# Kernel optimization log

Hardware: AMD Instinct MI355X
Metric: run time of the kernel (lower is better)

## Reference

```python
import jax, jax.numpy as jnp
import numpy as np

# dims (see shape_source)
B, N, P, H, M, E, HOPS = 512, 102, 12, 256, 4, 3, 2
C_CLIP = 10.0   # logit clipping constant params['C']
T = 1.0         # temperature params['T']
NEG = -1e9


def setup_inputs() -> dict:
    key = jax.random.key(0)
    ks = jax.random.split(key, 18)
    s = 0.08  # uniform init range as in _initialize_weights, use scaled normals
    inp = {
        "node_features": jax.random.normal(ks[0], (B, N, P), jnp.float32),
        "adjacency": jax.random.uniform(ks[1], (B, E, N, N), jnp.float32),  # per-edge-cat weighted adjacency
        "mask": jax.random.randint(ks[2], (B, N), 0, 2).astype(jnp.int32),  # 1 = already scheduled / forbidden
        # encoder params
        "W_emb": jax.random.normal(ks[3], (P, H), jnp.float32) * s,
        "W_rel": jax.random.normal(ks[4], (HOPS, E, H, H), jnp.float32) * s / np.sqrt(H),
        "W_self": jax.random.normal(ks[5], (HOPS, H, H), jnp.float32) * s / np.sqrt(H),
        # multi-head glimpse params (Vec / W_q / W_ref per head)
        "Vec": jax.random.normal(ks[6], (M, H, H), jnp.float32) * s,
        "W_q": jax.random.normal(ks[7], (M, 3 * H, H), jnp.float32) * s,
        "W_ref": jax.random.normal(ks[8], (M, H, H), jnp.float32) * s,
        "W_mh": jax.random.normal(ks[9], (M * H, H), jnp.float32) * s,  # multi_head_embedding
        # final pointer params
        "Vec2": jax.random.normal(ks[10], (H,), jnp.float32) * s,
        "W_q2": jax.random.normal(ks[11], (H, H), jnp.float32) * s,
        "W_ref2": jax.random.normal(ks[12], (H, H), jnp.float32) * s,
        # learned decoder seed vectors
        "dec_input": jax.random.normal(ks[13], (H,), jnp.float32) * s,
        "v_1": jax.random.normal(ks[14], (H,), jnp.float32) * s,
    }
    return inp


def reference(node_features, adjacency, mask, W_emb, W_rel, W_self, Vec, W_q,
              W_ref, W_mh, Vec2, W_q2, W_ref2, dec_input, v_1):
    # ---- encoder: linear embedding + HOPS of relational (per-edge-category) message passing ----
    h = jnp.einsum('bnp,ph->bnh', node_features, W_emb)            # [B,N,H]
    for hop in range(HOPS):
        msg = jnp.einsum('benm,bmh->benh', adjacency, h)           # gather neighbors per edge cat
        h = jax.nn.relu(jnp.einsum('benh,ehk->bnk', msg, W_rel[hop])
                        + jnp.einsum('bnh,hk->bnk', h, W_self[hop]))
    enc = h                                                         # [B,N,H]

    # ---- decoder query: cat(graph readout, learned dec_input, learned v_1) -> 3H ----
    enc_mean = enc.mean(axis=1)                                     # [B,H]
    q_cat = jnp.concatenate([enc_mean,
                             jnp.broadcast_to(dec_input, (B, H)),
                             jnp.broadcast_to(v_1, (B, H))], axis=-1)  # [B,3H]

    # ---- multi-head additive (Bahdanau) glimpse: per-head Vec/W_q/W_ref tanh scoring ----
    q = jnp.einsum('bf,mfh->bmh', q_cat, W_q)                       # [B,M,H]
    r = jnp.einsum('bnh,mhk->bmnk', enc, W_ref)                     # [B,M,N,H]
    u = jnp.einsum('bmnh,mhk->bmnk', jnp.tanh(q[:, :, None, :] + r), Vec)
    scores = u.sum(axis=-1)                                         # [B,M,N]
    scores = jnp.where(mask[:, None, :] > 0, NEG, scores)
    a = jax.nn.softmax(scores, axis=-1)
    ctx = jnp.einsum('bmn,bnh->bmh', a, enc).reshape(B, M * H)
    query2 = ctx @ W_mh                                             # [B,H]

    # ---- final pointer head (Vec2 / W_q2 / W_ref2) ----
    u2 = jnp.einsum('h,bnh->bn', Vec2,
                    jnp.tanh((query2 @ W_q2)[:, None, :] + jnp.einsum('bnh,hk->bnk', enc, W_ref2)))
    u2 = C_CLIP * jnp.tanh(u2)                                      # logit clipping
    u2 = jnp.where(mask > 0, NEG, u2)
    log_p = jax.nn.log_softmax(u2 / T, axis=-1)                     # [B,N]
    return log_p
```

## Files before the change

kernel.cpp:

```cpp
#include <hip/hip_runtime.h>
#include <hip/hip_bf16.h>

#define B 512
#define N 102
#define Pdim 12
#define H 256
#define M 4
#define E 3
#define NEG (-1e9f)
#define RT 52224
#define NN 10404

typedef __hip_bfloat16 bf16;
typedef __attribute__((ext_vector_type(8))) short short8;
typedef __attribute__((ext_vector_type(4))) float f32x4;
typedef __attribute__((ext_vector_type(16))) float f32x16;

__device__ __forceinline__ float b2f(bf16 v) { return __bfloat162float(v); }
__device__ __forceinline__ bf16 f2b(float v) { return __float2bfloat16(v); }
__device__ __forceinline__ short f2bs(float v) {
    bf16 t = __float2bfloat16(v);
    return *reinterpret_cast<short*>(&t);
}
__device__ __forceinline__ float fast_tanh(float x) {
    float e = __expf(2.f * x);
    return 1.f - 2.f * __builtin_amdgcn_rcpf(e + 1.f);
}
__device__ __forceinline__ void gload_lds4(const unsigned int* g, unsigned int* l) {
    __builtin_amdgcn_global_load_lds(
        (const __attribute__((address_space(1))) unsigned int*)g,
        (__attribute__((address_space(3))) unsigned int*)l, 4, 0, 0);
}

__global__ __launch_bounds__(256) void wt_prep(const float* __restrict__ Wrel,
                                               const float* __restrict__ Wself,
                                               const float* __restrict__ Wref,
                                               const float* __restrict__ Wref2,
                                               const float* __restrict__ Wmh,
                                               const float* __restrict__ Wq2,
                                               const float* __restrict__ W_q,
                                               const float* __restrict__ Vec,
                                               const float* __restrict__ W_emb,
                                               const float* __restrict__ dec,
                                               const float* __restrict__ v1,
                                               const float* __restrict__ adj,
                                               short* __restrict__ wfrag,
                                               short* __restrict__ wrefT,
                                               short* __restrict__ wref2T,
                                               short* __restrict__ wmh_bf,
                                               short* __restrict__ wq2_bf,
                                               short* __restrict__ wq_bf,
                                               short* __restrict__ wembf,
                                               short* __restrict__ adjp,
                                               float* __restrict__ qconst,
                                               float* __restrict__ vsum) {
    int bid = blockIdx.x;
    int tid = threadIdx.x;
    __shared__ short tl[1024 * 17];
    if (bid >= 3652) {
        int be = bid - 3652;
        const float* src = adj + (size_t)be * NN;
        short* dst = adjp + (size_t)be * (112 * 128);
        for (int i = tid; i < 112 * 128; i += 256) {
            int n = i >> 7, m = i & 127;
            short v = 0;
            if (n < N && m < N) v = f2bs(src[n * N + m]);
            dst[i] = v;
        }
        return;
    }
    if (bid < 32) {
        int hop = bid >> 4, ct = bid & 15;
        for (int i = tid; i < 16384; i += 256) {
            int k = i >> 4, c0 = i & 15;
            int c = ct * 16 + c0;
            float v;
            if (k < 768) v = Wrel[(((size_t)hop * E + (k >> 8)) * H + (k & 255)) * H + c];
            else         v = Wself[((size_t)hop * H + (k - 768)) * H + c];
            tl[k * 17 + c0] = f2bs(v);
        }
        __syncthreads();
        short8* outp = (short8*)wfrag + (size_t)(hop * 16 + ct) * 2048;
        for (int i = tid; i < 2048; i += 256) {
            int ks = i >> 6, lq = i & 63;
            int c0 = lq & 15, kb = (lq >> 4) * 8;
            short8 v;
#pragma unroll
            for (int j = 0; j < 8; ++j) v[j] = tl[(ks * 32 + kb + j) * 17 + c0];
            outp[i] = v;
        }
        return;
    }
    if (bid >= 3648) {
        int m = bid - 3648, hh = tid;
        __shared__ float dls[H], vls[H];
        dls[hh] = dec[hh];
        vls[hh] = v1[hh];
        __syncthreads();
        const float* Wm = W_q + (size_t)m * (3 * H) * H;
        float s = 0.f;
        for (int f = 0; f < H; ++f)
            s += dls[f] * Wm[(H + f) * H + hh] + vls[f] * Wm[(2 * H + f) * H + hh];
        qconst[m * H + hh] = s;
        float vs = 0.f;
        const float* Vr = Vec + ((size_t)m * H + hh) * H;
        for (int k = 0; k < H; ++k) vs += Vr[k];
        vsum[m * H + hh] = vs;
        return;
    }
    int idx = 524288 + (bid - 32) * 256 + tid;
    if (idx < 786432) {
        int r = idx - 524288;
        int row = r >> 8, k = r & 255;
        int m = row >> 8, c = row & 255;
        wrefT[r] = f2bs(Wref[((size_t)m * H + k) * H + c]);
    } else if (idx < 851968) {
        int r = idx - 786432;
        int c = r >> 8, k = r & 255;
        wref2T[r] = f2bs(Wref2[k * H + c]);
    } else if (idx < 1114112) {
        int r = idx - 851968;
        wmh_bf[r] = f2bs(Wmh[r]);
    } else if (idx < 1179648) {
        int r = idx - 1114112;
        wq2_bf[r] = f2bs(Wq2[r]);
    } else if (idx < 1441792) {
        int r = idx - 1179648;
        int m = r >> 16, fh = r & 65535;
        wq_bf[r] = f2bs(W_q[(size_t)m * 768 * 256 + fh]);
    } else if (idx < 1449984) {
        int r = idx - 1441792;
        int ct = r >> 9, lq = (r >> 3) & 63, j = r & 7;
        int c = ct * 16 + (lq & 15), k = (lq >> 4) * 8 + j;
        wembf[r] = (k < Pdim) ? f2bs(W_emb[k * H + c]) : (short)0;
    }
}

#define HP 264
#define YP2 136
#define ASP 136
__global__ __launch_bounds__(512, 2) void enc_fused(const float* __restrict__ nf,
                                                    const short* __restrict__ wembf,
                                                    const short* __restrict__ adjp,
                                                    const short* __restrict__ wfragp,
                                                    bf16* __restrict__ enc_out,
                                                    float* __restrict__ mean_out) {
    int b = blockIdx.x;
    int tid = threadIdx.x;
    int w = tid >> 6;
    int l = tid & 63;
    int cg = l & 15;
    int rg = l >> 4;
    int ct0 = 2 * w, ct1 = ct0 + 1;

    __shared__ short hS[112 * HP];
    __shared__ short YtS[256 * YP2];
    __shared__ short AsS[112 * ASP];

    const short8 z8 = {0, 0, 0, 0, 0, 0, 0, 0};
    for (int i = tid; i < 10 * 32; i += 512) {
        int n = 102 + (i >> 5), g = i & 31;
        *(short8*)(&hS[n * HP + g * 8]) = z8;
    }
    {
        int c = tid >> 1, g = 14 + (tid & 1);
        *(short8*)(&YtS[c * YP2 + g * 8]) = z8;
    }

    {
        const short8* we8 = (const short8*)wembf;
        short8 bfe0 = we8[ct0 * 64 + l];
        short8 bfe1 = we8[ct1 * 64 + l];
#pragma unroll
        for (int nt = 0; nt < 7; ++nt) {
            int row = nt * 16 + cg;
            short8 afr = z8;
            if (row < 102 && rg < 2) {
                const float* src = nf + ((size_t)b * N + row) * Pdim + rg * 8;
                f32x4 v0 = *(const f32x4*)src;
                afr[0] = f2bs(v0[0]); afr[1] = f2bs(v0[1]);
                afr[2] = f2bs(v0[2]); afr[3] = f2bs(v0[3]);
                if (rg == 0) {
                    f32x4 v1 = *(const f32x4*)(src + 4);
                    afr[4] = f2bs(v1[0]); afr[5] = f2bs(v1[1]);
                    afr[6] = f2bs(v1[2]); afr[7] = f2bs(v1[3]);
                }
            }
            f32x4 d0 = (f32x4){0.f, 0.f, 0.f, 0.f}, d1 = d0;
            d0 = __builtin_amdgcn_mfma_f32_16x16x32_bf16(afr, bfe0, d0, 0, 0, 0);
            d1 = __builtin_amdgcn_mfma_f32_16x16x32_bf16(afr, bfe1, d1, 0, 0, 0);
#pragma unroll
            for (int r = 0; r < 4; ++r) {
                int n = nt * 16 + rg * 4 + r;
                hS[n * HP + ct0 * 16 + cg] = f2bs(d0[r]);
                hS[n * HP + ct1 * 16 + cg] = f2bs(d1[r]);
            }
        }
    }
    __syncthreads();

    for (int hop = 0; hop < 2; ++hop) {
        const short8* wf8 = ((const short8*)wfragp) + (size_t)hop * 32768;
        f32x4 hacc0[7], hacc1[7];
#pragma unroll
        for (int j = 0; j < 7; ++j) {
            hacc0[j] = (f32x4){0.f, 0.f, 0.f, 0.f};
            hacc1[j] = hacc0[j];
        }

        for (int estep = 0; estep < E; ++estep) {
            int e = hop ? (2 - estep) : estep;
            if (!(hop == 1 && estep == 0)) {
                const short* Abase = adjp + (size_t)(b * E + e) * 14336;
#pragma unroll
                for (int j = 0; j < 14; ++j) {
                    int n = w * 14 + j;
                    const unsigned int* gsrc = (const unsigned int*)(Abase + n * 128) + l;
                    gload_lds4(gsrc, (unsigned int*)&AsS[n * ASP]);
                }
            }
            if (estep == 0) {
#pragma unroll
                for (int ks = 0; ks < 8; ++ks) {
                    short8 wfs0 = wf8[(ct0 * 32 + 24 + ks) * 64 + l];
                    short8 wfs1 = wf8[(ct1 * 32 + 24 + ks) * 64 + l];
#pragma unroll
                    for (int nt = 0; nt < 7; ++nt) {
                        short8 hf = *(const short8*)(&hS[(nt * 16 + cg) * HP + ks * 32 + rg * 8]);
                        hacc0[nt] = __builtin_amdgcn_mfma_f32_16x16x32_bf16(hf, wfs0, hacc0[nt], 0, 0, 0);
                        hacc1[nt] = __builtin_amdgcn_mfma_f32_16x16x32_bf16(hf, wfs1, hacc1[nt], 0, 0, 0);
                    }
                }
            }
            f32x4 g0[7], g1[7];
#pragma unroll
            for (int j = 0; j < 7; ++j) {
                g0[j] = (f32x4){0.f, 0.f, 0.f, 0.f};
                g1[j] = g0[j];
            }
#pragma unroll
            for (int ks = 0; ks < 8; ++ks) {
                short8 wfa0 = wf8[(ct0 * 32 + e * 8 + ks) * 64 + l];
                short8 wfa1 = wf8[(ct1 * 32 + e * 8 + ks) * 64 + l];
#pragma unroll
                for (int mt = 0; mt < 7; ++mt) {
                    short8 hf = *(const short8*)(&hS[(mt * 16 + cg) * HP + ks * 32 + rg * 8]);
                    g0[mt] = __builtin_amdgcn_mfma_f32_16x16x32_bf16(wfa0, hf, g0[mt], 0, 0, 0);
                    g1[mt] = __builtin_amdgcn_mfma_f32_16x16x32_bf16(wfa1, hf, g1[mt], 0, 0, 0);
                }
            }
#pragma unroll
            for (int mt = 0; mt < 7; ++mt)
#pragma unroll
                for (int r = 0; r < 4; ++r) {
                    int c0 = ct0 * 16 + rg * 4 + r;
                    int c1 = ct1 * 16 + rg * 4 + r;
                    YtS[c0 * YP2 + mt * 16 + cg] = f2bs(g0[mt][r]);
                    YtS[c1 * YP2 + mt * 16 + cg] = f2bs(g1[mt][r]);
                }
            __syncthreads();
#pragma unroll
            for (int ks = 0; ks < 4; ++ks) {
                short8 yf0 = *(const short8*)(&YtS[(ct0 * 16 + cg) * YP2 + (ks * 4 + rg) * 8]);
                short8 yf1 = *(const short8*)(&YtS[(ct1 * 16 + cg) * YP2 + (ks * 4 + rg) * 8]);
#pragma unroll
                for (int nt = 0; nt < 7; ++nt) {
                    short8 af = *(const short8*)(&AsS[(nt * 16 + cg) * ASP + ks * 32 + rg * 8]);
                    hacc0[nt] = __builtin_amdgcn_mfma_f32_16x16x32_bf16(af, yf0, hacc0[nt], 0, 0, 0);
                    hacc1[nt] = __builtin_amdgcn_mfma_f32_16x16x32_bf16(af, yf1, hacc1[nt], 0, 0, 0);
                }
            }
            __syncthreads();
        }
#pragma unroll
        for (int nt = 0; nt < 7; ++nt)
#pragma unroll
            for (int r = 0; r < 4; ++r) {
                int n = nt * 16 + rg * 4 + r;
                float v0 = hacc0[nt][r], v1 = hacc1[nt][r];
                hS[n * HP + ct0 * 16 + cg] = f2bs(v0 > 0.f ? v0 : 0.f);
                hS[n * HP + ct1 * 16 + cg] = f2bs(v1 > 0.f ? v1 : 0.f);
            }
        __syncthreads();
    }

    short* ho = (short*)enc_out;
    for (int i = tid; i < 102 * 32; i += 512) {
        int n = i >> 5, g = i & 31;
        *(short8*)(ho + ((size_t)b * N + n) * H + g * 8) = *(const short8*)(&hS[n * HP + g * 8]);
    }
    {
        float* partf = (float*)AsS;
        int c = tid & 255, qq = tid >> 8;
        float s = 0.f;
        for (int n = qq; n < N; n += 2) s += b2f(*(const bf16*)&hS[n * HP + c]);
        partf[qq * 256 + c] = s;
        __syncthreads();
        if (tid < 256)
            mean_out[(size_t)b * H + tid] = (partf[tid] + partf[256 + tid]) * (1.f / (float)N);
    }
}

__global__ __launch_bounds__(256, 2) void head2_mfma(const bf16* __restrict__ X,
                                                     const short* __restrict__ WT,
                                                     const float* __restrict__ qb, int qbs,
                                                     const float* __restrict__ vsb,
                                                     float* __restrict__ outp, int obs,
                                                     int mcnt) {
    int rt = blockIdx.x;
    int r0 = rt * 128;
    int tid = threadIdx.x;
    int w = tid >> 6, l = tid & 63;
    int lr = l & 31;
    int lh = l >> 5;
    __shared__ short Xs[128 * 256];
    __shared__ float qls[12 * 256];
    __shared__ float part[4][128];

    const short* Xp = (const short*)X;
#pragma unroll
    for (int i = 0; i < 16; ++i) {
        int id = tid + i * 256;
        int r = id >> 5, g = id & 31;
        short8 v = *(const short8*)(Xp + (size_t)(r0 + r) * H + g * 8);
        *(short8*)((char*)Xs + r * 512 + ((g ^ (r & 7)) * 16)) = v;
    }
    int b_base = r0 / N;
    for (int i = tid; i < 3 * mcnt * 256; i += 256) {
        int boff = i / (mcnt * 256);
        int rem = i - boff * (mcnt * 256);
        int m = rem >> 8, c = rem & 255;
        int bb = b_base + boff;
        if (bb > B - 1) bb = B - 1;
        qls[(boff * mcnt + m) * 256 + c] = qb[(size_t)bb * qbs + m * H + c];
    }
    __syncthreads();

    int swz = lr & 7;
    for (int m = 0; m < mcnt; ++m) {
        const short8* w8 = (const short8*)(WT + (size_t)m * H * H);
        int cbase = w * 64;
        short8 afr0[16], afr1[16];
#pragma unroll
        for (int ks = 0; ks < 16; ++ks) {
            afr0[ks] = w8[(size_t)(cbase + lr) * 32 + ks * 2 + lh];
            afr1[ks] = w8[(size_t)(cbase + 32 + lr) * 32 + ks * 2 + lh];
        }
        float vsl[32];
#pragma unroll
        for (int j = 0; j < 16; ++j) {
            int cl = (j & 3) + 8 * (j >> 2) + 4 * lh;
            vsl[j]      = vsb[m * H + w * 64 + cl];
            vsl[16 + j] = vsb[m * H + w * 64 + 32 + cl];
        }
        for (int t = 0; t < 4; ++t) {
            f32x16 acc0, acc1;
#pragma unroll
            for (int j = 0; j < 16; ++j) { acc0[j] = 0.f; acc1[j] = 0.f; }
            const char* xbase = (const char*)Xs + (t * 32 + lr) * 512;
#pragma unroll
            for (int ks = 0; ks < 16; ++ks) {
                short8 bx = *(const short8*)(xbase + (((2 * ks + lh) ^ swz) * 16));
                acc0 = __builtin_amdgcn_mfma_f32_32x32x16_bf16(afr0[ks], bx, acc0, 0, 0, 0);
                acc1 = __builtin_amdgcn_mfma_f32_32x32x16_bf16(afr1[ks], bx, acc1, 0, 0, 0);
            }
            int r = r0 + t * 32 + lr;
            int b = r / N;
            int boff = b - b_base;
            const float* qrow = &qls[(boff * mcnt + m) * 256];
            float s = 0.f;
#pragma unroll
            for (int j = 0; j < 16; ++j) {
                int cl = (j & 3) + 8 * (j >> 2) + 4 * lh;
                float x0 = qrow[w * 64 + cl] + acc0[j];
                s += fast_tanh(x0) * vsl[j];
                float x1 = qrow[w * 64 + 32 + cl] + acc1[j];
                s += fast_tanh(x1) * vsl[16 + j];
            }
            s += __shfl_xor(s, 32, 64);
            if (l < 32) part[w][t * 32 + lr] = s;
        }
        __syncthreads();
        if (tid < 128) {
            int r = r0 + tid;
            int b = r / N, n = r - b * N;
            outp[(size_t)b * obs + m * N + n] = part[0][tid] + part[1][tid] + part[2][tid] + part[3][tid];
        }
        __syncthreads();
    }
}

__global__ __launch_bounds__(256) void q_k(const float* __restrict__ enc_mean,
                                           const short* __restrict__ wq_bf,
                                           const float* __restrict__ qconst,
                                           float* __restrict__ qbuf) {
    int bid = blockIdx.x;
    int b = bid >> 2, m = bid & 3;
    int hh = threadIdx.x;
    __shared__ float em[H];
    em[hh] = enc_mean[(size_t)b * H + hh];
    __syncthreads();
    const bf16* Wm = (const bf16*)(wq_bf + (size_t)m * 65536);
    float s = qconst[m * H + hh];
    for (int f = 0; f < H; ++f) s += em[f] * b2f(Wm[f * H + hh]);
    qbuf[((size_t)b * M + m) * H + hh] = s;
}

__global__ __launch_bounds__(256) void dec_mid_k(const float* __restrict__ scores,
                                                 const int* __restrict__ mask,
                                                 const bf16* __restrict__ enc,
                                                 const short* __restrict__ wmh,
                                                 const short* __restrict__ wq2,
                                                 float* __restrict__ q2) {
    int b = blockIdx.x;
    int tid = threadIdx.x;
    int w = tid >> 6;
    int l = tid & 63;
    __shared__ short hEnc[102 * 264];
    __shared__ float a[M][112];
    __shared__ float red[M];
    __shared__ float cx[M * H];
    __shared__ float qy[H];

    const short* ep = (const short*)enc;
    for (int i = tid; i < 102 * 32; i += 256) {
        int n = i >> 5, g = i & 31;
        *(short8*)(&hEnc[n * 264 + g * 8]) = *(const short8*)(ep + ((size_t)b * N + n) * H + g * 8);
    }
    for (int i = tid; i < M * 112; i += 256) {
        int m = i / 112, n = i % 112;
        float s = NEG;
        if (n < N) s = (mask[(size_t)b * N + n] > 0) ? NEG : scores[((size_t)b * M + m) * N + n];
        a[m][n] = s;
    }
    __syncthreads();
    {
        float v = a[w][l];
        float v2 = (l + 64 < 112) ? a[w][l + 64] : NEG;
        v = fmaxf(v, v2);
        v = fmaxf(v, __shfl_xor(v, 32, 64));
        v = fmaxf(v, __shfl_xor(v, 16, 64));
        v = fmaxf(v, __shfl_xor(v, 8, 64));
        v = fmaxf(v, __shfl_xor(v, 4, 64));
        v = fmaxf(v, __shfl_xor(v, 2, 64));
        v = fmaxf(v, __shfl_xor(v, 1, 64));
        float mx = __shfl(v, 0, 64);
        float e0 = __expf(a[w][l] - mx);
        float e1 = (l + 64 < 112) ? __expf(a[w][l + 64] - mx) : 0.f;
        a[w][l] = e0;
        if (l + 64 < 112) a[w][l + 64] = e1;
        float sv = e0 + e1;
        sv += __shfl_xor(sv, 32, 64);
        sv += __shfl_xor(sv, 16, 64);
        sv += __shfl_xor(sv, 8, 64);
        sv += __shfl_xor(sv, 4, 64);
        sv += __shfl_xor(sv, 2, 64);
        sv += __shfl_xor(sv, 1, 64);
        if (l == 0) red[w] = __builtin_amdgcn_rcpf(sv);
    }
    __syncthreads();
    float c0 = 0.f, c1 = 0.f, c2 = 0.f, c3 = 0.f;
    for (int n = 0; n < N; ++n) {
        float e = b2f(*(const bf16*)&hEnc[n * 264 + tid]);
        c0 += a[0][n] * e;
        c1 += a[1][n] * e;
        c2 += a[2][n] * e;
        c3 += a[3][n] * e;
    }
    cx[0 * H + tid] = c0 * red[0];
    cx[1 * H + tid] = c1 * red[1];
    cx[2 * H + tid] = c2 * red[2];
    cx[3 * H + tid] = c3 * red[3];
    __syncthreads();
    const bf16* wm = (const bf16*)wmh;
    float acc = 0.f;
    for (int j = 0; j < M * H; ++j) acc += cx[j] * b2f(wm[(size_t)j * H + tid]);
    qy[tid] = acc;
    __syncthreads();
    const bf16* w2 = (const bf16*)wq2;
    float acc2 = 0.f;
    for (int k = 0; k < H; ++k) acc2 += qy[k] * b2f(w2[(size_t)k * H + tid]);
    q2[(size_t)b * H + tid] = acc2;
}

__global__ __launch_bounds__(128) void final_out_k(const float* __restrict__ u2,
                                                   const int* __restrict__ mask,
                                                   float* __restrict__ out) {
    int b = blockIdx.x;
    int tid = threadIdx.x;
    __shared__ float a[128];
    __shared__ float red[2];
    float u = NEG;
    if (tid < N) {
        u = 10.f * fast_tanh(u2[(size_t)b * N + tid]);
        if (mask[(size_t)b * N + tid] > 0) u = NEG;
    }
    a[tid] = u;
    __syncthreads();
    if (tid < 64) {
        float v = fmaxf(a[tid], a[tid + 64]);
        v = fmaxf(v, __shfl_xor(v, 32, 64));
        v = fmaxf(v, __shfl_xor(v, 16, 64));
        v = fmaxf(v, __shfl_xor(v, 8, 64));
        v = fmaxf(v, __shfl_xor(v, 4, 64));
        v = fmaxf(v, __shfl_xor(v, 2, 64));
        v = fmaxf(v, __shfl_xor(v, 1, 64));
        if (tid == 0) red[0] = v;
    }
    __syncthreads();
    float mx = red[0];
    float ev = (tid < N) ? __expf(u - mx) : 0.f;
    a[tid] = ev;
    __syncthreads();
    if (tid < 64) {
        float v = a[tid] + a[tid + 64];
        v += __shfl_xor(v, 32, 64);
        v += __shfl_xor(v, 16, 64);
        v += __shfl_xor(v, 8, 64);
        v += __shfl_xor(v, 4, 64);
        v += __shfl_xor(v, 2, 64);
        v += __shfl_xor(v, 1, 64);
        if (tid == 0) red[1] = logf(v);
    }
    __syncthreads();
    if (tid < N) out[(size_t)b * N + tid] = (u - mx) - red[1];
}

extern "C" void kernel_launch(void* const* d_in, const int* in_sizes, int n_in,
                              void* d_out, int out_size, void* d_ws, size_t ws_size,
                              hipStream_t stream) {
    const float* nf     = (const float*)d_in[0];
    const float* adj    = (const float*)d_in[1];
    const int*   mask   = (const int*)d_in[2];
    const float* W_emb  = (const float*)d_in[3];
    const float* W_rel  = (const float*)d_in[4];
    const float* W_self = (const float*)d_in[5];
    const float* Vec    = (const float*)d_in[6];
    const float* W_q    = (const float*)d_in[7];
    const float* W_ref  = (const float*)d_in[8];
    const float* W_mh   = (const float*)d_in[9];
    const float* Vec2   = (const float*)d_in[10];
    const float* W_q2   = (const float*)d_in[11];
    const float* W_ref2 = (const float*)d_in[12];
    const float* dec    = (const float*)d_in[13];
    const float* v_1    = (const float*)d_in[14];
    float* out = (float*)d_out;

    char* p = (char*)d_ws;
    size_t off = 0;
    auto alloc = [&](size_t bytes) -> char* {
        char* q = p + off;
        off += (bytes + 255) & ~(size_t)255;
        return q;
    };
    bf16* hA      = (bf16*)alloc((size_t)RT * H * sizeof(bf16));
    short* adjp   = (short*)alloc((size_t)B * E * 112 * 128 * sizeof(short));
    short* wfrag  = (short*)alloc(524288 * sizeof(short));
    short* wrefT  = (short*)alloc(262144 * sizeof(short));
    short* wref2T = (short*)alloc(65536 * sizeof(short));
    short* wmh_bf = (short*)alloc(262144 * sizeof(short));
    short* wq2_bf = (short*)alloc(65536 * sizeof(short));
    short* wq_bf  = (short*)alloc(262144 * sizeof(short));
    short* wembf  = (short*)alloc(8192 * sizeof(short));
    float* enc_mean = (float*)alloc((size_t)B * H * sizeof(float));
    float* qconst   = (float*)alloc((size_t)M * H * sizeof(float));
    float* vsumb    = (float*)alloc((size_t)M * H * sizeof(float));
    float* qbuf     = (float*)alloc((size_t)B * M * H * sizeof(float));
    float* scoresb  = (float*)alloc((size_t)B * M * N * sizeof(float));
    float* q2b      = (float*)alloc((size_t)B * H * sizeof(float));
    float* u2b      = (float*)alloc((size_t)B * N * sizeof(float));

    wt_prep<<<5188, 256, 0, stream>>>(W_rel, W_self, W_ref, W_ref2, W_mh, W_q2,
                                      W_q, Vec, W_emb, dec, v_1, adj,
                                      wfrag, wrefT, wref2T, wmh_bf, wq2_bf, wq_bf, wembf,
                                      adjp, qconst, vsumb);

    enc_fused<<<B, 512, 0, stream>>>(nf, wembf, adjp, wfrag, hA, enc_mean);

    const bf16* enc = hA;

    q_k<<<B * M, 256, 0, stream>>>(enc_mean, wq_bf, qconst, qbuf);
    head2_mfma<<<RT / 128, 256, 0, stream>>>(enc, wrefT, qbuf, M * H, vsumb, scoresb, M * N, M);
    dec_mid_k<<<B, 256, 0, stream>>>(scoresb, mask, enc, wmh_bf, wq2_bf, q2b);
    head2_mfma<<<RT / 128, 256, 0, stream>>>(enc, wref2T, q2b, H, Vec2, u2b, N, 1);
    final_out_k<<<B, 128, 0, stream>>>(u2b, mask, out);
}
```

Before: 266.2 us.

## Fuse decoder glimpse, context, pointer head and log-softmax into one per-batch kernel

Replaces four decoder kernels (two head2_mfma launches, dec_mid_k, final_out_k) with one dec_fused kernel, one block per batch element. The encoder tile is loaded into LDS once and reused for the multi-head scoring MFMAs, the context reduction and the final pointer MFMAs, which removes the intermediate scores, q2 and u2 round-trips through global memory and three launches. In exchange, each block pads 102 rows to 128, so a quarter of the MFMA work is wasted. The grid is also 512 blocks instead of 408, and the serial per-thread W_mh/W_q2 matvecs now sit inside the same kernel as the MFMA work.

Measured after the change: 282.2 us. 6.0% more time.

```diff
diff --git a/kernel.cpp b/kernel.cpp
--- a/kernel.cpp
+++ b/kernel.cpp
@@ -301,95 +301,6 @@
     }
 }
 
-__global__ __launch_bounds__(256, 2) void head2_mfma(const bf16* __restrict__ X,
-                                                     const short* __restrict__ WT,
-                                                     const float* __restrict__ qb, int qbs,
-                                                     const float* __restrict__ vsb,
-                                                     float* __restrict__ outp, int obs,
-                                                     int mcnt) {
-    int rt = blockIdx.x;
-    int r0 = rt * 128;
-    int tid = threadIdx.x;
-    int w = tid >> 6, l = tid & 63;
-    int lr = l & 31;
-    int lh = l >> 5;
-    __shared__ short Xs[128 * 256];
-    __shared__ float qls[12 * 256];
-    __shared__ float part[4][128];
-
-    const short* Xp = (const short*)X;
-#pragma unroll
-    for (int i = 0; i < 16; ++i) {
-        int id = tid + i * 256;
-        int r = id >> 5, g = id & 31;
-        short8 v = *(const short8*)(Xp + (size_t)(r0 + r) * H + g * 8);
-        *(short8*)((char*)Xs + r * 512 + ((g ^ (r & 7)) * 16)) = v;
-    }
-    int b_base = r0 / N;
-    for (int i = tid; i < 3 * mcnt * 256; i += 256) {
-        int boff = i / (mcnt * 256);
-        int rem = i - boff * (mcnt * 256);
-        int m = rem >> 8, c = rem & 255;
-        int bb = b_base + boff;
-        if (bb > B - 1) bb = B - 1;
-        qls[(boff * mcnt + m) * 256 + c] = qb[(size_t)bb * qbs + m * H + c];
-    }
-    __syncthreads();
-
-    int swz = lr & 7;
-    for (int m = 0; m < mcnt; ++m) {
-        const short8* w8 = (const short8*)(WT + (size_t)m * H * H);
-        int cbase = w * 64;
-        short8 afr0[16], afr1[16];
-#pragma unroll
-        for (int ks = 0; ks < 16; ++ks) {
-            afr0[ks] = w8[(size_t)(cbase + lr) * 32 + ks * 2 + lh];
-            afr1[ks] = w8[(size_t)(cbase + 32 + lr) * 32 + ks * 2 + lh];
-        }
-        float vsl[32];
-#pragma unroll
-        for (int j = 0; j < 16; ++j) {
-            int cl = (j & 3) + 8 * (j >> 2) + 4 * lh;
-            vsl[j]      = vsb[m * H + w * 64 + cl];
-            vsl[16 + j] = vsb[m * H + w * 64 + 32 + cl];
-        }
-        for (int t = 0; t < 4; ++t) {
-            f32x16 acc0, acc1;
-#pragma unroll
-            for (int j = 0; j < 16; ++j) { acc0[j] = 0.f; acc1[j] = 0.f; }
-            const char* xbase = (const char*)Xs + (t * 32 + lr) * 512;
-#pragma unroll
-            for (int ks = 0; ks < 16; ++ks) {
-                short8 bx = *(const short8*)(xbase + (((2 * ks + lh) ^ swz) * 16));
-                acc0 = __builtin_amdgcn_mfma_f32_32x32x16_bf16(afr0[ks], bx, acc0, 0, 0, 0);
-                acc1 = __builtin_amdgcn_mfma_f32_32x32x16_bf16(afr1[ks], bx, acc1, 0, 0, 0);
-            }
-            int r = r0 + t * 32 + lr;
-            int b = r / N;
-            int boff = b - b_base;
-            const float* qrow = &qls[(boff * mcnt + m) * 256];
-            float s = 0.f;
-#pragma unroll
-            for (int j = 0; j < 16; ++j) {
-                int cl = (j & 3) + 8 * (j >> 2) + 4 * lh;
-                float x0 = qrow[w * 64 + cl] + acc0[j];
-                s += fast_tanh(x0) * vsl[j];
-                float x1 = qrow[w * 64 + 32 + cl] + acc1[j];
-                s += fast_tanh(x1) * vsl[16 + j];
-            }
-            s += __shfl_xor(s, 32, 64);
-            if (l < 32) part[w][t * 32 + lr] = s;
-        }
-        __syncthreads();
-        if (tid < 128) {
-            int r = r0 + tid;
-            int b = r / N, n = r - b * N;
-            outp[(size_t)b * obs + m * N + n] = part[0][tid] + part[1][tid] + part[2][tid] + part[3][tid];
-        }
-        __syncthreads();
-    }
-}
-
 __global__ __launch_bounds__(256) void q_k(const float* __restrict__ enc_mean,
                                            const short* __restrict__ wq_bf,
                                            const float* __restrict__ qconst,
@@ -406,38 +317,94 @@
     qbuf[((size_t)b * M + m) * H + hh] = s;
 }
 
-__global__ __launch_bounds__(256) void dec_mid_k(const float* __restrict__ scores,
-                                                 const int* __restrict__ mask,
-                                                 const bf16* __restrict__ enc,
-                                                 const short* __restrict__ wmh,
-                                                 const short* __restrict__ wq2,
-                                                 float* __restrict__ q2) {
+__global__ __launch_bounds__(256, 2) void dec_fused(const bf16* __restrict__ X,
+                                                    const short* __restrict__ wrefT,
+                                                    const short* __restrict__ wref2T,
+                                                    const float* __restrict__ qb,
+                                                    const float* __restrict__ vsb,
+                                                    const short* __restrict__ wmh,
+                                                    const short* __restrict__ wq2,
+                                                    const float* __restrict__ Vec2,
+                                                    const int* __restrict__ mask,
+                                                    float* __restrict__ out) {
     int b = blockIdx.x;
     int tid = threadIdx.x;
-    int w = tid >> 6;
-    int l = tid & 63;
-    __shared__ short hEnc[102 * 264];
-    __shared__ float a[M][112];
+    int w = tid >> 6, l = tid & 63;
+    int lr = l & 31, lh = l >> 5;
+    __shared__ short Xs[128 * 256];
+    __shared__ float qls[M * 256];
+    __shared__ float part[4][128];
+    __shared__ float a[M][128];
     __shared__ float red[M];
-    __shared__ float cx[M * H];
-    __shared__ float qy[H];
-
-    const short* ep = (const short*)enc;
-    for (int i = tid; i < 102 * 32; i += 256) {
-        int n = i >> 5, g = i & 31;
-        *(short8*)(&hEnc[n * 264 + g * 8]) = *(const short8*)(ep + ((size_t)b * N + n) * H + g * 8);
-    }
-    for (int i = tid; i < M * 112; i += 256) {
-        int m = i / 112, n = i % 112;
-        float s = NEG;
-        if (n < N) s = (mask[(size_t)b * N + n] > 0) ? NEG : scores[((size_t)b * M + m) * N + n];
-        a[m][n] = s;
-    }
-    __syncthreads();
-    {
-        float v = a[w][l];
-        float v2 = (l + 64 < 112) ? a[w][l + 64] : NEG;
-        v = fmaxf(v, v2);
+    __shared__ float cx[M * 256];
+    __shared__ float qy[256];
+    __shared__ float q2s[256];
+    __shared__ float fr[2];
+
+    const short8 z8 = {0, 0, 0, 0, 0, 0, 0, 0};
+    const short* Xp = (const short*)X;
+#pragma unroll
+    for (int i = 0; i < 16; ++i) {
+        int id = tid + i * 256;
+        int r = id >> 5, g = id & 31;
+        short8 v = z8;
+        if (r < N) v = *(const short8*)(Xp + ((size_t)b * N + r) * H + g * 8);
+        *(short8*)((char*)Xs + r * 512 + ((g ^ (r & 7)) * 16)) = v;
+    }
+    for (int i = tid; i < M * 256; i += 256) qls[i] = qb[(size_t)b * (M * H) + i];
+    __syncthreads();
+
+    int swz = lr & 7;
+    for (int m = 0; m < M; ++m) {
+        const short8* w8 = (const short8*)(wrefT + (size_t)m * H * H);
+        int cbase = w * 64;
+        short8 afr0[16], afr1[16];
+#pragma unroll
+        for (int ks = 0; ks < 16; ++ks) {
+            afr0[ks] = w8[(size_t)(cbase + lr) * 32 + ks * 2 + lh];
+            afr1[ks] = w8[(size_t)(cbase + 32 + lr) * 32 + ks * 2 + lh];
+        }
+        float vsl[32];
+#pragma unroll
+        for (int j = 0; j < 16; ++j) {
+            int cl = (j & 3) + 8 * (j >> 2) + 4 * lh;
+            vsl[j]      = vsb[m * H + w * 64 + cl];
+            vsl[16 + j] = vsb[m * H + w * 64 + 32 + cl];
+        }
+        const float* qrow = &qls[m * 256];
+        for (int t = 0; t < 4; ++t) {
+            f32x16 acc0, acc1;
+#pragma unroll
+            for (int j = 0; j < 16; ++j) { acc0[j] = 0.f; acc1[j] = 0.f; }
+            const char* xbase = (const char*)Xs + (t * 32 + lr) * 512;
+#pragma unroll
+            for (int ks = 0; ks < 16; ++ks) {
+                short8 bx = *(const short8*)(xbase + (((2 * ks + lh) ^ swz) * 16));
+                acc0 = __builtin_amdgcn_mfma_f32_32x32x16_bf16(afr0[ks], bx, acc0, 0, 0, 0);
+                acc1 = __builtin_amdgcn_mfma_f32_32x32x16_bf16(afr1[ks], bx, acc1, 0, 0, 0);
+            }
+            float s = 0.f;
+#pragma unroll
+            for (int j = 0; j < 16; ++j) {
+                int cl = (j & 3) + 8 * (j >> 2) + 4 * lh;
+                s += fast_tanh(qrow[w * 64 + cl] + acc0[j]) * vsl[j];
+                s += fast_tanh(qrow[w * 64 + 32 + cl] + acc1[j]) * vsl[16 + j];
+            }
+            s += __shfl_xor(s, 32, 64);
+            if (l < 32) part[w][t * 32 + lr] = s;
+        }
+        __syncthreads();
+        if (tid < 128) {
+            int n = tid;
+            float s = part[0][n] + part[1][n] + part[2][n] + part[3][n];
+            if (n >= N || mask[(size_t)b * N + (n < N ? n : 0)] > 0) s = NEG;
+            a[m][n] = s;
+        }
+        __syncthreads();
+    }
+
+    {
+        float v = fmaxf(a[w][l], a[w][l + 64]);
         v = fmaxf(v, __shfl_xor(v, 32, 64));
         v = fmaxf(v, __shfl_xor(v, 16, 64));
         v = fmaxf(v, __shfl_xor(v, 8, 64));
@@ -446,9 +413,9 @@
         v = fmaxf(v, __shfl_xor(v, 1, 64));
         float mx = __shfl(v, 0, 64);
         float e0 = __expf(a[w][l] - mx);
-        float e1 = (l + 64 < 112) ? __expf(a[w][l + 64] - mx) : 0.f;
+        float e1 = __expf(a[w][l + 64] - mx);
         a[w][l] = e0;
-        if (l + 64 < 112) a[w][l + 64] = e1;
+        a[w][l + 64] = e1;
         float sv = e0 + e1;
         sv += __shfl_xor(sv, 32, 64);
         sv += __shfl_xor(sv, 16, 64);
@@ -459,71 +426,112 @@
         if (l == 0) red[w] = __builtin_amdgcn_rcpf(sv);
     }
     __syncthreads();
-    float c0 = 0.f, c1 = 0.f, c2 = 0.f, c3 = 0.f;
-    for (int n = 0; n < N; ++n) {
-        float e = b2f(*(const bf16*)&hEnc[n * 264 + tid]);
-        c0 += a[0][n] * e;
-        c1 += a[1][n] * e;
-        c2 += a[2][n] * e;
-        c3 += a[3][n] * e;
-    }
-    cx[0 * H + tid] = c0 * red[0];
-    cx[1 * H + tid] = c1 * red[1];
-    cx[2 * H + tid] = c2 * red[2];
-    cx[3 * H + tid] = c3 * red[3];
-    __syncthreads();
-    const bf16* wm = (const bf16*)wmh;
-    float acc = 0.f;
-    for (int j = 0; j < M * H; ++j) acc += cx[j] * b2f(wm[(size_t)j * H + tid]);
-    qy[tid] = acc;
-    __syncthreads();
-    const bf16* w2 = (const bf16*)wq2;
-    float acc2 = 0.f;
-    for (int k = 0; k < H; ++k) acc2 += qy[k] * b2f(w2[(size_t)k * H + tid]);
-    q2[(size_t)b * H + tid] = acc2;
-}
-
-__global__ __launch_bounds__(128) void final_out_k(const float* __restrict__ u2,
-                                                   const int* __restrict__ mask,
-                                                   float* __restrict__ out) {
-    int b = blockIdx.x;
-    int tid = threadIdx.x;
-    __shared__ float a[128];
-    __shared__ float red[2];
-    float u = NEG;
-    if (tid < N) {
-        u = 10.f * fast_tanh(u2[(size_t)b * N + tid]);
-        if (mask[(size_t)b * N + tid] > 0) u = NEG;
-    }
-    a[tid] = u;
+    {
+        int g = tid >> 3, bo = (tid & 7) * 2;
+        float c0 = 0.f, c1 = 0.f, c2 = 0.f, c3 = 0.f;
+        for (int n = 0; n < N; ++n) {
+            float e = b2f(*(const bf16*)((const char*)Xs + n * 512 + ((g ^ (n & 7)) << 4) + bo));
+            c0 += a[0][n] * e;
+            c1 += a[1][n] * e;
+            c2 += a[2][n] * e;
+            c3 += a[3][n] * e;
+        }
+        cx[0 * 256 + tid] = c0 * red[0];
+        cx[1 * 256 + tid] = c1 * red[1];
+        cx[2 * 256 + tid] = c2 * red[2];
+        cx[3 * 256 + tid] = c3 * red[3];
+    }
+    __syncthreads();
+    {
+        const bf16* wm = (const bf16*)wmh;
+        float acc = 0.f;
+        for (int j = 0; j < M * H; ++j) acc += cx[j] * b2f(wm[(size_t)j * H + tid]);
+        qy[tid] = acc;
+    }
+    __syncthreads();
+    {
+        const bf16* w2 = (const bf16*)wq2;
+        float acc2 = 0.f;
+        for (int k = 0; k < H; ++k) acc2 += qy[k] * b2f(w2[(size_t)k * H + tid]);
+        q2s[tid] = acc2;
+    }
+    __syncthreads();
+
+    {
+        const short8* w8 = (const short8*)wref2T;
+        int cbase = w * 64;
+        short8 afr0[16], afr1[16];
+#pragma unroll
+        for (int ks = 0; ks < 16; ++ks) {
+            afr0[ks] = w8[(size_t)(cbase + lr) * 32 + ks * 2 + lh];
+            afr1[ks] = w8[(size_t)(cbase + 32 + lr) * 32 + ks * 2 + lh];
+        }
+        float vsl[32];
+#pragma unroll
+        for (int j = 0; j < 16; ++j) {
+            int cl = (j & 3) + 8 * (j >> 2) + 4 * lh;
+            vsl[j]      = Vec2[w * 64 + cl];
+            vsl[16 + j] = Vec2[w * 64 + 32 + cl];
+        }
+        for (int t = 0; t < 4; ++t) {
+            f32x16 acc0, acc1;
+#pragma unroll
+            for (int j = 0; j < 16; ++j) { acc0[j] = 0.f; acc1[j] = 0.f; }
+            const char* xbase = (const char*)Xs + (t * 32 + lr) * 512;
+#pragma unroll
+            for (int ks = 0; ks < 16; ++ks) {
+                short8 bx = *(const short8*)(xbase + (((2 * ks + lh) ^ swz) * 16));
+                acc0 = __builtin_amdgcn_mfma_f32_32x32x16_bf16(afr0[ks], bx, acc0, 0, 0, 0);
+                acc1 = __builtin_amdgcn_mfma_f32_32x32x16_bf16(afr1[ks], bx, acc1, 0, 0, 0);
+            }
+            float s = 0.f;
+#pragma unroll
+            for (int j = 0; j < 16; ++j) {
+                int cl = (j & 3) + 8 * (j >> 2) + 4 * lh;
+                s += fast_tanh(q2s[w * 64 + cl] + acc0[j]) * vsl[j];
+                s += fast_tanh(q2s[w * 64 + 32 + cl] + acc1[j]) * vsl[16 + j];
+            }
+            s += __shfl_xor(s, 32, 64);
+            if (l < 32) part[w][t * 32 + lr] = s;
+        }
+        __syncthreads();
+        if (tid < 128) {
+            int n = tid;
+            float u = NEG;
+            if (n < N && mask[(size_t)b * N + n] <= 0) {
+                float u2 = part[0][n] + part[1][n] + part[2][n] + part[3][n];
+                u = 10.f * fast_tanh(u2);
+            }
+            a[0][n] = u;
+        }
+    }
     __syncthreads();
     if (tid < 64) {
-        float v = fmaxf(a[tid], a[tid + 64]);
+        float v = fmaxf(a[0][tid], a[0][tid + 64]);
         v = fmaxf(v, __shfl_xor(v, 32, 64));
         v = fmaxf(v, __shfl_xor(v, 16, 64));
         v = fmaxf(v, __shfl_xor(v, 8, 64));
         v = fmaxf(v, __shfl_xor(v, 4, 64));
         v = fmaxf(v, __shfl_xor(v, 2, 64));
         v = fmaxf(v, __shfl_xor(v, 1, 64));
-        if (tid == 0) red[0] = v;
-    }
-    __syncthreads();
-    float mx = red[0];
-    float ev = (tid < N) ? __expf(u - mx) : 0.f;
-    a[tid] = ev;
+        if (tid == 0) fr[0] = v;
+    }
+    __syncthreads();
+    float mx = fr[0];
+    if (tid < 128) part[0][tid] = __expf(a[0][tid] - mx);
     __syncthreads();
     if (tid < 64) {
-        float v = a[tid] + a[tid + 64];
+        float v = part[0][tid] + part[0][tid + 64];
         v += __shfl_xor(v, 32, 64);
         v += __shfl_xor(v, 16, 64);
         v += __shfl_xor(v, 8, 64);
         v += __shfl_xor(v, 4, 64);
         v += __shfl_xor(v, 2, 64);
         v += __shfl_xor(v, 1, 64);
-        if (tid == 0) red[1] = logf(v);
-    }
-    __syncthreads();
-    if (tid < N) out[(size_t)b * N + tid] = (u - mx) - red[1];
+        if (tid == 0) fr[1] = logf(v);
+    }
+    __syncthreads();
+    if (tid < N) out[(size_t)b * N + tid] = (a[0][tid] - mx) - fr[1];
 }
 
 extern "C" void kernel_launch(void* const* d_in, const int* in_sizes, int n_in,
@@ -566,9 +574,6 @@
     float* qconst   = (float*)alloc((size_t)M * H * sizeof(float));
     float* vsumb    = (float*)alloc((size_t)M * H * sizeof(float));
     float* qbuf     = (float*)alloc((size_t)B * M * H * sizeof(float));
-    float* scoresb  = (float*)alloc((size_t)B * M * N * sizeof(float));
-    float* q2b      = (float*)alloc((size_t)B * H * sizeof(float));
-    float* u2b      = (float*)alloc((size_t)B * N * sizeof(float));
 
     wt_prep<<<5188, 256, 0, stream>>>(W_rel, W_self, W_ref, W_ref2, W_mh, W_q2,
                                       W_q, Vec, W_emb, dec, v_1, adj,
@@ -580,8 +585,6 @@
     const bf16* enc = hA;
 
     q_k<<<B * M, 256, 0, stream>>>(enc_mean, wq_bf, qconst, qbuf);
-    head2_mfma<<<RT / 128, 256, 0, stream>>>(enc, wrefT, qbuf, M * H, vsumb, scoresb, M * N, M);
-    dec_mid_k<<<B, 256, 0, stream>>>(scoresb, mask, enc, wmh_bf, wq2_bf, q2b);
-    head2_mfma<<<RT / 128, 256, 0, stream>>>(enc, wref2T, q2b, H, Vec2, u2b, N, 1);
-    final_out_k<<<B, 128, 0, stream>>>(u2b, mask, out);
-}
+    dec_fused<<<B, 256, 0, stream>>>(enc, wrefT, wref2T, qbuf, vsumb,
+                                     wmh_bf, wq2_bf, Vec2, mask, out);
+}
```
